# Kernel tuning notes

Measured on AMD Instinct MI355X. Metric: run time of the kernel, lower is better.

## Reference

```python
import jax, jax.numpy as jnp
import numpy as np
from jax import lax

# ---- static config (from BasePllay_2 / AdTopoLayer(out_features=50, T=25, m0=0.2, lims=[[224,0],[0,224]], K_max=2, p=0)) ----
H = W = 28
G = H * W
T = 25
K_MAX = 2
M0 = 0.2
OUT_FEATURES = 50
B = 32
TSEQ = jnp.linspace(0.0, 100.0, T)  # fixed landscape sample grid (covers DTM value range)

# static grid geometry from lims=[[224,0],[0,224]]
_xs = np.linspace(224.0, 0.0, H)
_ys = np.linspace(0.0, 224.0, W)
_pts = np.stack(np.meshgrid(_xs, _ys, indexing="ij"), -1).reshape(G, 2)
_d = np.sqrt(((_pts[:, None] - _pts[None]) ** 2).sum(-1))
_sidx = np.argsort(_d, axis=-1)
SDIST = jnp.asarray(np.take_along_axis(_d, _sidx, -1), jnp.float32)  # [G,G] sorted distances per grid point
SIDX = jnp.asarray(_sidx.astype(np.int32))                            # [G,G] static distance-sort order

# 4-connectivity neighbor table for the cubical (pixel) grid, -1 = invalid
_ii = np.arange(G).reshape(H, W)
_nb = np.full((H, W, 4), -1, np.int32)
_nb[1:, :, 0] = _ii[:-1, :]
_nb[:-1, :, 1] = _ii[1:, :]
_nb[:, 1:, 2] = _ii[:, :-1]
_nb[:, :-1, 3] = _ii[:, 1:]
NBR = jnp.asarray(_nb.reshape(G, 4))


def dtm(w):
    """Weighted distance-to-measure (r=2) on the fixed grid. w: [B,G] nonneg -> [B,G]."""
    sw = w[:, SIDX]                               # [B,G,G] weights in distance order
    cw = jnp.cumsum(sw, -1)
    d2 = SDIST ** 2
    cwd = jnp.cumsum(sw * d2[None], -1)
    bound = M0 * w.sum(-1)                        # [B]
    k = jnp.argmax(cw >= bound[:, None, None], -1)  # [B,G] first index reaching mass bound
    km1 = jnp.maximum(k - 1, 0)
    take = lambda a, i: jnp.take_along_axis(a, i[..., None], -1)[..., 0]
    has_prev = k > 0
    cw_p = jnp.where(has_prev, take(cw, km1), 0.0)
    cwd_p = jnp.where(has_prev, take(cwd, km1), 0.0)
    dk2 = d2[jnp.arange(G)[None, :], k]           # [B,G]
    val = (cwd_p + (bound[:, None] - cw_p) * dk2) / bound[:, None]
    return jnp.sqrt(jnp.maximum(val, 0.0))


def pd0(vals):
    """0-dim sublevel-set persistence of vals on the pixel grid (union-find, elder rule).
    Returns (births[G], deaths[G]); non-merging pixels yield zero-persistence pairs,
    essential components die at the max filtration value."""
    order = jnp.argsort(vals).astype(jnp.int32)
    rank = jnp.zeros(G, jnp.int32).at[order].set(jnp.arange(G, dtype=jnp.int32))

    def find(parent, i):
        return lax.while_loop(lambda j: parent[j] != j, lambda j: parent[j], i)

    def step(s, carry):
        parent, death = carry
        p = order[s]
        best = p
        for t in range(4):  # unrolled over the 4 grid neighbors (static)
            q = NBR[p, t]
            ok = (q >= 0) & (rank[jnp.maximum(q, 0)] < s)  # neighbor already inserted
            r = find(parent, jnp.where(ok, q, p))
            merge = ok & (r != best)
            r_old = rank[r] < rank[best]
            older = jnp.where(r_old, r, best)
            younger = jnp.where(r_old, best, r)
            widx = jnp.where(merge, younger, G)   # slot G is a dummy
            parent = parent.at[widx].set(older)
            death = death.at[widx].set(p)         # younger component dies at pixel p
            best = jnp.where(merge, older, best)
        return parent, death

    parent0 = jnp.arange(G + 1, dtype=jnp.int32)
    death0 = jnp.full(G + 1, -1, jnp.int32)
    _, death = lax.fori_loop(0, G, step, (parent0, death0))
    d = death[:G]
    deaths = jnp.where(d >= 0, vals[jnp.maximum(d, 0)], vals.max())
    return vals, deaths


def landscape(births, deaths):
    """K_MAX persistence landscapes sampled at TSEQ. [B,G] -> [B, K_MAX*T]."""
    tb = TSEQ[None, :, None] - births[:, None, :]   # [B,T,G]
    td = deaths[:, None, :] - TSEQ[None, :, None]
    tent = jnp.maximum(jnp.minimum(tb, td), 0.0)
    topk = lax.top_k(tent, K_MAX)[0]                # [B,T,K]
    return jnp.transpose(topk, (0, 2, 1)).reshape(births.shape[0], K_MAX * T)


def _forward(x, w_land, b_land, w_fc, b_fc):
    w = x.reshape(x.shape[0], -1)          # nn.Flatten: pixel intensities as measure weights
    v = dtm(w)                             # [B,G]
    births, deaths = jax.vmap(pd0)(v)
    feats = landscape(births, deaths)      # [B, 50]
    xt = feats @ w_land.T + b_land         # AdTopoLayer output [B, out_features]
    signal = jnp.abs(lax.stop_gradient(xt)).sum(0)   # torch: x.detach().abs().sum(0)
    out = jnp.maximum(xt, 0.0) @ w_fc.T + b_fc       # fc(relu(x))
    return out, signal

_forward_jit = jax.jit(_forward)


def setup_inputs() -> dict:
    key = jax.random.key(0)
    k = jax.random.split(key, 4)
    x = jax.random.uniform(k[0], (B, 1, H, W), jnp.float32)  # image-like nonneg weights
    w_land = jax.random.normal(k[1], (OUT_FEATURES, K_MAX * T), jnp.float32) * 0.1
    b_land = jnp.zeros((OUT_FEATURES,), jnp.float32)
    w_fc = jax.random.normal(k[2], (10, OUT_FEATURES), jnp.float32) * 0.1
    b_fc = jnp.zeros((10,), jnp.float32)
    return {"x": x, "w_land": w_land, "b_land": b_land, "w_fc": w_fc, "b_fc": b_fc}


def reference(x, w_land, b_land, w_fc, b_fc):
    return _forward_jit(x, w_land, b_land, w_fc, b_fc)
```

## Files before the change

### kernel.cpp

```cpp
#include <hip/hip_runtime.h>
#include <math.h>

#define H28 28
#define G784 784
#define BATCH 32
#define NOFF 3025
#define NOFFP 3072
#define NKEY 1459
#define TPTS 25
#define KMAX 2
#define NFEAT 50
#define OUTF 50
#define NCLS 10

#define NBX 16
#define BT 512
#define BT2 512
#define NWAVE (BT2 / 64)
#define HS 2048
#define EMAX 1024

struct OffPair { unsigned ij; float d2; };
struct OffTab  { OffPair e[NOFFP]; };

constexpr double csqrt(double x) {
  double r = x * 0.5 + 1.0;
  for (int i = 0; i < 20; i++) r = 0.5 * (r + x / r);
  return r;
}

constexpr OffTab make_offtab() {
  OffTab t{};
  int start[NKEY] = {};
  for (int i = 0; i < NOFF; i++) {
    int di = i / 55 - 27, dj = i % 55 - 27;
    start[di * di + dj * dj]++;
  }
  int run = 0;
  for (int k = 0; k < NKEY; k++) { int h = start[k]; start[k] = run; run += h; }
  for (int i = 0; i < NOFF; i++) {
    int di = i / 55 - 27, dj = i % 55 - 27;
    int key = di * di + dj * dj;
    int pos = start[key]++;
    float sd = (key == 0) ? 0.0f : (float)(csqrt((double)key) * (224.0 / 27.0));
    t.e[pos].ij = ((unsigned)(di & 0xffff)) | (((unsigned)(dj & 0xffff)) << 16);
    t.e[pos].d2 = sd * sd;
  }
  for (int i = NOFF; i < NOFFP; i++) { t.e[i].ij = 0x00640064u; t.e[i].d2 = 0.f; }
  return t;
}

__device__ constexpr OffTab OFFTAB = make_offtab();

__device__ __forceinline__ float wave_iscan_f32(float x) {
  int t;
  t = __builtin_amdgcn_update_dpp(0, __float_as_int(x), 0x111, 0xf, 0xf, true);
  x += __int_as_float(t);
  t = __builtin_amdgcn_update_dpp(0, __float_as_int(x), 0x112, 0xf, 0xf, true);
  x += __int_as_float(t);
  t = __builtin_amdgcn_update_dpp(0, __float_as_int(x), 0x114, 0xf, 0xf, true);
  x += __int_as_float(t);
  t = __builtin_amdgcn_update_dpp(0, __float_as_int(x), 0x118, 0xf, 0xf, true);
  x += __int_as_float(t);
  t = __builtin_amdgcn_update_dpp(0, __float_as_int(x), 0x142, 0xa, 0xf, true);
  x += __int_as_float(t);
  t = __builtin_amdgcn_update_dpp(0, __float_as_int(x), 0x143, 0xc, 0xf, true);
  x += __int_as_float(t);
  return x;
}

__global__ __launch_bounds__(BT) void dtm_kernel(const float* __restrict__ x,
                                                 float* __restrict__ v,
                                                 int* __restrict__ done_ctr) {
  __shared__ float w_s[G784];
  __shared__ float red[BT];

  const int tid = threadIdx.x;
  const int b   = blockIdx.x;
  const int bx  = blockIdx.y;

  if (b == 0 && bx == 0 && tid == 0) *done_ctr = 0;

  float ps = 0.f;
  for (int i = tid; i < G784; i += BT) {
    float wv = x[b * G784 + i];
    w_s[i] = wv;
    ps += wv;
  }
  red[tid] = ps;
  __syncthreads();
  if (tid < 256) red[tid] += red[tid + 256];
  __syncthreads();
  if (tid < 128) red[tid] += red[tid + 128];
  __syncthreads();
  if (tid < 64)  red[tid] += red[tid + 64];
  __syncthreads();
  if (tid < 64) {
    float vv = red[tid];
    vv += __shfl_down(vv, 32);
    vv += __shfl_down(vv, 16);
    vv += __shfl_down(vv, 8);
    vv += __shfl_down(vv, 4);
    vv += __shfl_down(vv, 2);
    vv += __shfl_down(vv, 1);
    if (tid == 0) red[0] = vv;
  }
  __syncthreads();
  const float bound = 0.2f * red[0];

  const int wave = tid >> 6;
  const int lane = tid & 63;
  const int slot = bx * 8 + wave;

  for (int g = slot; g < G784; g += NBX * 8) {
    const int i1 = g / H28, j1 = g % H28;
    float cw = 0.f, cwd = 0.f;
    float cwp = 0.f, cwdp = 0.f, dk2 = 0.f;
    bool crossed = false;
    int o = lane;
    unsigned ij = OFFTAB.e[o].ij;
    float d2v   = OFFTAB.e[o].d2;
    for (int base = 0; base < NOFFP && !crossed; base += 64) {
      int onext = o + 64;
      if (onext >= NOFFP) onext = o;
      const unsigned ij_n = OFFTAB.e[onext].ij;
      const float    d2_n = OFFTAB.e[onext].d2;
      const int di = (short)(ij & 0xffffu);
      const int dj = (short)(ij >> 16);
      const int i2 = i1 + di, j2 = j1 + dj;
      const bool inb = ((unsigned)i2 < (unsigned)H28) & ((unsigned)j2 < (unsigned)H28);
      const float wv = inb ? w_s[i2 * H28 + j2] : 0.f;
      const float wd = wv * d2v;
      const float psw = wave_iscan_f32(wv);
      const float psd = wave_iscan_f32(wd);
      const unsigned long long mask = __ballot(cw + psw >= bound);
      if (mask) {
        const int f = __ffsll((unsigned long long)mask) - 1;
        const float psw_f = __shfl(psw, f);
        const float w_f   = __shfl(wv, f);
        const float psd_f = __shfl(psd, f);
        const float wd_f  = __shfl(wd, f);
        dk2  = __shfl(d2v, f);
        cwp  = cw + (psw_f - w_f);
        cwdp = cwd + (psd_f - wd_f);
        crossed = true;
      } else {
        cw  += __int_as_float(__builtin_amdgcn_readlane(__float_as_int(psw), 63));
        cwd += __int_as_float(__builtin_amdgcn_readlane(__float_as_int(psd), 63));
      }
      ij = ij_n; d2v = d2_n; o = onext;
    }
    const float val = (cwdp + (bound - cwp) * dk2) / bound;
    if (lane == 0) v[b * G784 + g] = sqrtf(fmaxf(val, 0.f));
  }
}

__device__ __forceinline__ unsigned long long pix_key(const float* val_s, int p) {
  return (((unsigned long long)__float_as_uint(val_s[p])) << 10) | (unsigned)p;
}

__global__ __launch_bounds__(BT2) void pd0_kernel(const float* __restrict__ v,
                                                  float* __restrict__ feats,
                                                  int* __restrict__ done_ctr,
                                                  const float* __restrict__ w_land,
                                                  const float* __restrict__ b_land,
                                                  const float* __restrict__ w_fc,
                                                  const float* __restrict__ b_fc,
                                                  float* __restrict__ out) {
  __shared__ float val_s[G784];
  __shared__ int   ptr_s[G784];
  __shared__ int   parent[G784];
  __shared__ unsigned rank_s[G784];
  __shared__ unsigned claims[G784];
  __shared__ float deathv[G784];
  __shared__ int   mlist[G784];
  __shared__ unsigned long long oldkey[G784];
  __shared__ unsigned htag[HS];
  __shared__ unsigned long long hval[HS];
  __shared__ unsigned long long edges[EMAX];
  __shared__ float redf[NWAVE];
  __shared__ float wt1[NWAVE][TPTS];
  __shared__ float wt2[NWAVE][TPTS];
  __shared__ int   mcnt_sh, ecnt_sh, last_sh;
  __shared__ float vmax_sh;
  __shared__ float f_s[BATCH * NFEAT];
  __shared__ float xt_s[BATCH * OUTF];

  const int tid = threadIdx.x;
  const int b   = blockIdx.x;
  const int wave = tid >> 6;
  const int lane = tid & 63;
  if (tid == 0) { mcnt_sh = 0; ecnt_sh = 0; }

  for (int i = tid; i < HS; i += BT2) { htag[i] = 0u; hval[i] = ~0ULL; }

  float pm = -1e30f;
  for (int i = tid; i < G784; i += BT2) {
    float xv = v[b * G784 + i];
    val_s[i] = xv;
    pm = fmaxf(pm, xv);
    rank_s[i] = 0u;
    claims[i] = 0xFFFFFFFFu;
  }
  pm = fmaxf(pm, __shfl_down(pm, 32));
  pm = fmaxf(pm, __shfl_down(pm, 16));
  pm = fmaxf(pm, __shfl_down(pm, 8));
  pm = fmaxf(pm, __shfl_down(pm, 4));
  pm = fmaxf(pm, __shfl_down(pm, 2));
  pm = fmaxf(pm, __shfl_down(pm, 1));
  if (lane == 0) redf[wave] = pm;
  __syncthreads();
  if (tid == 0) {
    float m = redf[0];
    for (int w = 1; w < NWAVE; w++) m = fmaxf(m, redf[w]);
    vmax_sh = m;
  }
  __syncthreads();
  const float vmax = vmax_sh;

  for (int p = tid; p < G784; p += BT2) {
    unsigned long long kp = pix_key(val_s, p);
    int i = p / H28, j = p % H28;
    int nbs[4];
    nbs[0] = (i > 0)       ? p - H28 : -1;
    nbs[1] = (i < H28 - 1) ? p + H28 : -1;
    nbs[2] = (j > 0)       ? p - 1   : -1;
    nbs[3] = (j < H28 - 1) ? p + 1   : -1;
    int best = p;
    unsigned long long bk = kp;
    for (int t = 0; t < 4; t++) {
      int q = nbs[t];
      if (q >= 0) {
        unsigned long long kq = pix_key(val_s, q);
        if (kq < bk) { bk = kq; best = q; }
      }
    }
    ptr_s[p]  = best;
    parent[p] = p;
    deathv[p] = vmax;
    if (best == p) {
      oldkey[p] = kp;
      int mi = atomicAdd(&mcnt_sh, 1);
      mlist[mi] = p;
    }
  }
  __syncthreads();

  for (int r = 0; r < 5; r++) {
    for (int p = tid; p < G784; p += BT2) {
      int a = ptr_s[p];
      a = ptr_s[a];
      a = ptr_s[a];
      a = ptr_s[a];
      ptr_s[p] = a;
    }
    __syncthreads();
  }

  for (int p = tid; p < G784; p += BT2) {
    unsigned long long kp = pix_key(val_s, p);
    int i = p / H28, j = p % H28;
    int nbs[4];
    nbs[0] = (i > 0)       ? p - H28 : -1;
    nbs[1] = (i < H28 - 1) ? p + H28 : -1;
    nbs[2] = (j > 0)       ? p - 1   : -1;
    nbs[3] = (j < H28 - 1) ? p + 1   : -1;
    int bp = ptr_s[p];
    for (int t = 0; t < 4; t++) {
      int q = nbs[t];
      if (q >= 0) {
        unsigned long long kq = pix_key(val_s, q);
        int bq = ptr_s[q];
        if (kq < kp && bq != bp) {
          unsigned long long key =
              (((unsigned long long)__float_as_uint(val_s[p])) << 32) |
              (((unsigned long long)(unsigned)p) << 22) |
              (((unsigned long long)(unsigned)t) << 20) |
              (((unsigned long long)(unsigned)bp) << 10) |
              ((unsigned long long)(unsigned)bq);
          unsigned lo = (bp < bq) ? (unsigned)bp : (unsigned)bq;
          unsigned hi = (bp < bq) ? (unsigned)bq : (unsigned)bp;
          unsigned pairid = (lo << 10) | hi;
          unsigned idx = (pairid * 2654435761u) >> 21;
          for (;;) {
            unsigned t0 = atomicCAS(&htag[idx], 0u, pairid + 1u);
            if (t0 == 0u || t0 == pairid + 1u) { atomicMin(&hval[idx], key); break; }
            idx = (idx + 1) & (HS - 1);
          }
        }
      }
    }
  }
  __syncthreads();

  for (int i = tid; i < HS; i += BT2) {
    if (htag[i]) {
      int e = atomicAdd(&ecnt_sh, 1);
      if (e < EMAX) edges[e] = hval[i];
    }
  }
  __syncthreads();
  const int ne   = (ecnt_sh < EMAX) ? ecnt_sh : EMAX;
  const int mcnt = mcnt_sh;

  if (ne > 1 && ne <= BT2) {
    unsigned long long e = (tid < ne) ? edges[tid] : ~0ULL;
    __syncthreads();
    for (int kk = 2; kk <= BT2; kk <<= 1) {
      const bool up = ((tid & kk) == 0);
      for (int jj = kk >> 1; jj >= 64; jj >>= 1) {
        edges[tid] = e;
        __syncthreads();
        unsigned long long p = edges[tid ^ jj];
        __syncthreads();
        const bool lower = ((tid & jj) == 0);
        const bool keepmin = (up == lower);
        e = keepmin ? ((e < p) ? e : p) : ((e > p) ? e : p);
      }
      int jj0 = (kk >> 1 < 32) ? (kk >> 1) : 32;
      for (int jj = jj0; jj >= 1; jj >>= 1) {
        unsigned long long p = __shfl_xor((long long)e, jj, 64);
        const bool lower = ((tid & jj) == 0);
        const bool keepmin = (up == lower);
        e = keepmin ? ((e < p) ? e : p) : ((e > p) ? e : p);
      }
    }
    edges[tid] = e;
    __syncthreads();
  } else if (ne > 1) {
    int n2 = 1;
    while (n2 < ne) n2 <<= 1;
    for (int i = ne + tid; i < n2; i += BT2) edges[i] = ~0ULL;
    __syncthreads();
    for (int kk = 2; kk <= n2; kk <<= 1) {
      for (int jj = kk >> 1; jj > 0; jj >>= 1) {
        for (int i = tid; i < n2; i += BT2) {
          int ixj = i ^ jj;
          if (ixj > i) {
            unsigned long long a = edges[i], c = edges[ixj];
            bool up = ((i & kk) == 0);
            if ((a > c) == up) { edges[i] = c; edges[ixj] = a; }
          }
        }
        __syncthreads();
      }
    }
  }

  if (wave == 0) {
    int merged = 0;
    const int target = mcnt - 1;
    for (int base = 0; base < ne && merged < target; base += 64) {
      const int idx = base + lane;
      bool unresolved = (idx < ne);
      const unsigned long long e = unresolved ? edges[idx] : 0ULL;
      const int A  = (int)((e >> 10) & 1023u);
      const int Bq = (int)(e & 1023u);
      const float ev = __uint_as_float((unsigned)(e >> 32));
      for (;;) {
        int rA = A, rB = Bq;
        if (unresolved) {
          int xx = A;
          for (;;) { int p1 = parent[xx]; if (p1 == xx) break;
                     int p2 = parent[p1]; parent[xx] = p2; xx = p2; }
          rA = xx;
          xx = Bq;
          for (;;) { int p1 = parent[xx]; if (p1 == xx) break;
                     int p2 = parent[p1]; parent[xx] = p2; xx = p2; }
          rB = xx;
        }
        bool crossing = unresolved && (rA != rB);
        if (unresolved && !crossing) unresolved = false;
        if (__ballot(crossing) == 0ULL) break;
        if (crossing) {
          atomicMin(&claims[rA], (unsigned)lane);
          atomicMin(&claims[rB], (unsigned)lane);
        }
        __threadfence_block();
        bool win = crossing && claims[rA] == (unsigned)lane
                            && claims[rB] == (unsigned)lane;
        __threadfence_block();
        if (crossing) { claims[rA] = 0xFFFFFFFFu; claims[rB] = 0xFFFFFFFFu; }
        if (win) {
          unsigned long long ka = oldkey[rA], kb = oldkey[rB];
          unsigned ra_ = rank_s[rA], rb_ = rank_s[rB];
          int big   = (ra_ > rb_) ? rA : ((rb_ > ra_) ? rB : ((rA < rB) ? rA : rB));
          int small = (big == rA) ? rB : rA;
          parent[small] = big;
          if (ra_ == rb_) rank_s[big] = ra_ + 1u;
          unsigned long long okmin = (ka < kb) ? ka : kb;
          unsigned long long okmax = (ka < kb) ? kb : ka;
          oldkey[big] = okmin;
          int dying = (int)(okmax & 1023u);
          deathv[dying] = ev;
          unresolved = false;
        }
        __threadfence_block();
        merged += (int)__popcll(__ballot(win));
        if (merged >= target) break;
      }
    }
  }
  __syncthreads();

  if (lane < TPTS) {
    float ti = (float)((double)lane * (100.0 / 24.0));
    float t1 = 0.f, t2 = 0.f;
    for (int ii = wave; ii < mcnt; ii += NWAVE) {
      int m = mlist[ii];
      float tent = fminf(ti - val_s[m], deathv[m] - ti);
      tent = fmaxf(tent, 0.f);
      if (tent > t1)      { t2 = t1; t1 = tent; }
      else if (tent > t2) { t2 = tent; }
    }
    wt1[wave][lane] = t1;
    wt2[wave][lane] = t2;
  }
  __syncthreads();
  if (wave == 0 && lane < TPTS) {
    float t1 = 0.f, t2 = 0.f;
    for (int w = 0; w < NWAVE; w++) {
      float a = wt1[w][lane], c = wt2[w][lane];
      if (a >= t1) { t2 = fmaxf(t1, c); t1 = a; }
      else         { t2 = fmaxf(t2, a); }
    }
    feats[b * NFEAT + lane]        = t1;
    feats[b * NFEAT + TPTS + lane] = t2;
  }

  __threadfence();
  __syncthreads();
  if (tid == 0) last_sh = (atomicAdd(done_ctr, 1) == BATCH - 1) ? 1 : 0;
  __syncthreads();
  if (!last_sh) return;
  __threadfence();

  for (int i = tid; i < BATCH * NFEAT; i += BT2) f_s[i] = feats[i];
  __syncthreads();
  for (int idx = tid; idx < BATCH * OUTF; idx += BT2) {
    int bb = idx / OUTF, ff = idx % OUTF;
    float acc = b_land[ff];
    const float* wr = w_land + ff * NFEAT;
    const float* fr = f_s + bb * NFEAT;
    for (int j = 0; j < NFEAT; j++) acc += fr[j] * wr[j];
    xt_s[idx] = acc;
  }
  __syncthreads();
  if (tid < OUTF) {
    float s = 0.f;
    for (int bb = 0; bb < BATCH; bb++) s += fabsf(xt_s[bb * OUTF + tid]);
    out[BATCH * NCLS + tid] = s;
  }
  for (int idx = tid; idx < BATCH * NCLS; idx += BT2) {
    int bb = idx / NCLS, cc = idx % NCLS;
    float acc = b_fc[cc];
    const float* wr = w_fc + cc * OUTF;
    const float* xr = xt_s + bb * OUTF;
    for (int ff = 0; ff < OUTF; ff++) acc += fmaxf(xr[ff], 0.f) * wr[ff];
    out[bb * NCLS + cc] = acc;
  }
}

extern "C" void kernel_launch(void* const* d_in, const int* in_sizes, int n_in,
                              void* d_out, int out_size, void* d_ws, size_t ws_size,
                              hipStream_t stream) {
  (void)in_sizes; (void)n_in; (void)out_size; (void)ws_size;
  const float* x      = (const float*)d_in[0];
  const float* w_land = (const float*)d_in[1];
  const float* b_land = (const float*)d_in[2];
  const float* w_fc   = (const float*)d_in[3];
  const float* b_fc   = (const float*)d_in[4];
  float* out   = (float*)d_out;
  float* v     = (float*)d_ws;
  float* feats = v + BATCH * G784;
  int*   done  = (int*)(feats + BATCH * NFEAT);

  dim3 g1(BATCH, NBX);
  dtm_kernel<<<g1, BT, 0, stream>>>(x, v, done);
  pd0_kernel<<<BATCH, BT2, 0, stream>>>(v, feats, done,
                                        w_land, b_land, w_fc, b_fc, out);
}
```

Before: 101.8 us.

## Fuse DTM and persistence kernels via per-batch last-block-done counters

Merges the DTM and pd0 kernels into one launch: each of the NBX blocks per batch item computes its share of DTM values, then a per-batch atomic counter elects the last finishing block to run the union-find persistence and landscape for that item. The goal is to drop the second kernel launch and the grid-wide wait between the stages, so persistence for finished items overlaps with DTM work on others. Counters are padded per batch and cleared with a memset launch instead of in-kernel. The large shared-memory footprint now applies to every DTM block, which may lower occupancy. The in-register bitonic sort path is also generalized to any power-of-two size up to the block size.

Result: slower. 173.7 us (+70.7%).

```diff
diff --git a/kernel.cpp b/kernel.cpp
--- a/kernel.cpp
+++ b/kernel.cpp
@@ -15,10 +15,10 @@
 
 #define NBX 16
 #define BT 512
-#define BT2 512
-#define NWAVE (BT2 / 64)
+#define NWAVE (BT / 64)
 #define HS 2048
 #define EMAX 1024
+#define CSTRIDE 16
 
 struct OffPair { unsigned ij; float d2; };
 struct OffTab  { OffPair e[NOFFP]; };
@@ -69,17 +69,45 @@
   return x;
 }
 
-__global__ __launch_bounds__(BT) void dtm_kernel(const float* __restrict__ x,
-                                                 float* __restrict__ v,
-                                                 int* __restrict__ done_ctr) {
+__device__ __forceinline__ unsigned long long pix_key(const float* val_s, int p) {
+  return (((unsigned long long)__float_as_uint(val_s[p])) << 10) | (unsigned)p;
+}
+
+__global__ __launch_bounds__(BT) void fused_kernel(const float* __restrict__ x,
+                                                   float* __restrict__ v,
+                                                   float* __restrict__ feats,
+                                                   int* __restrict__ done,
+                                                   const float* __restrict__ w_land,
+                                                   const float* __restrict__ b_land,
+                                                   const float* __restrict__ w_fc,
+                                                   const float* __restrict__ b_fc,
+                                                   float* __restrict__ out) {
   __shared__ float w_s[G784];
   __shared__ float red[BT];
-
-  const int tid = threadIdx.x;
-  const int b   = blockIdx.x;
-  const int bx  = blockIdx.y;
-
-  if (b == 0 && bx == 0 && tid == 0) *done_ctr = 0;
+  __shared__ float val_s[G784];
+  __shared__ int   ptr_s[G784];
+  __shared__ int   parent[G784];
+  __shared__ unsigned rank_s[G784];
+  __shared__ unsigned claims[G784];
+  __shared__ float deathv[G784];
+  __shared__ int   mlist[G784];
+  __shared__ unsigned long long oldkey[G784];
+  __shared__ unsigned htag[HS];
+  __shared__ unsigned long long hval[HS];
+  __shared__ unsigned long long edges[EMAX];
+  __shared__ float redf[NWAVE];
+  __shared__ float wt1[NWAVE][TPTS];
+  __shared__ float wt2[NWAVE][TPTS];
+  __shared__ int   mcnt_sh, ecnt_sh, winner_sh, last_sh;
+  __shared__ float vmax_sh;
+  __shared__ float f_s[BATCH * NFEAT];
+  __shared__ float xt_s[BATCH * OUTF];
+
+  const int tid  = threadIdx.x;
+  const int b    = blockIdx.x;
+  const int bx   = blockIdx.y;
+  const int wave = tid >> 6;
+  const int lane = tid & 63;
 
   float ps = 0.f;
   for (int i = tid; i < G784; i += BT) {
@@ -108,10 +136,7 @@
   __syncthreads();
   const float bound = 0.2f * red[0];
 
-  const int wave = tid >> 6;
-  const int lane = tid & 63;
   const int slot = bx * 8 + wave;
-
   for (int g = slot; g < G784; g += NBX * 8) {
     const int i1 = g / H28, j1 = g % H28;
     float cw = 0.f, cwd = 0.f;
@@ -153,49 +178,22 @@
     const float val = (cwdp + (bound - cwp) * dk2) / bound;
     if (lane == 0) v[b * G784 + g] = sqrtf(fmaxf(val, 0.f));
   }
-}
-
-__device__ __forceinline__ unsigned long long pix_key(const float* val_s, int p) {
-  return (((unsigned long long)__float_as_uint(val_s[p])) << 10) | (unsigned)p;
-}
-
-__global__ __launch_bounds__(BT2) void pd0_kernel(const float* __restrict__ v,
-                                                  float* __restrict__ feats,
-                                                  int* __restrict__ done_ctr,
-                                                  const float* __restrict__ w_land,
-                                                  const float* __restrict__ b_land,
-                                                  const float* __restrict__ w_fc,
-                                                  const float* __restrict__ b_fc,
-                                                  float* __restrict__ out) {
-  __shared__ float val_s[G784];
-  __shared__ int   ptr_s[G784];
-  __shared__ int   parent[G784];
-  __shared__ unsigned rank_s[G784];
-  __shared__ unsigned claims[G784];
-  __shared__ float deathv[G784];
-  __shared__ int   mlist[G784];
-  __shared__ unsigned long long oldkey[G784];
-  __shared__ unsigned htag[HS];
-  __shared__ unsigned long long hval[HS];
-  __shared__ unsigned long long edges[EMAX];
-  __shared__ float redf[NWAVE];
-  __shared__ float wt1[NWAVE][TPTS];
-  __shared__ float wt2[NWAVE][TPTS];
-  __shared__ int   mcnt_sh, ecnt_sh, last_sh;
-  __shared__ float vmax_sh;
-  __shared__ float f_s[BATCH * NFEAT];
-  __shared__ float xt_s[BATCH * OUTF];
-
-  const int tid = threadIdx.x;
-  const int b   = blockIdx.x;
-  const int wave = tid >> 6;
-  const int lane = tid & 63;
-  if (tid == 0) { mcnt_sh = 0; ecnt_sh = 0; }
-
-  for (int i = tid; i < HS; i += BT2) { htag[i] = 0u; hval[i] = ~0ULL; }
+
+  __threadfence();
+  __syncthreads();
+  if (tid == 0) {
+    int old = atomicAdd(&done[b * CSTRIDE], 1);
+    winner_sh = (old == NBX - 1) ? 1 : 0;
+    mcnt_sh = 0; ecnt_sh = 0;
+  }
+  __syncthreads();
+  if (!winner_sh) return;
+  __threadfence();
+
+  for (int i = tid; i < HS; i += BT) { htag[i] = 0u; hval[i] = ~0ULL; }
 
   float pm = -1e30f;
-  for (int i = tid; i < G784; i += BT2) {
+  for (int i = tid; i < G784; i += BT) {
     float xv = v[b * G784 + i];
     val_s[i] = xv;
     pm = fmaxf(pm, xv);
@@ -218,7 +216,7 @@
   __syncthreads();
   const float vmax = vmax_sh;
 
-  for (int p = tid; p < G784; p += BT2) {
+  for (int p = tid; p < G784; p += BT) {
     unsigned long long kp = pix_key(val_s, p);
     int i = p / H28, j = p % H28;
     int nbs[4];
@@ -247,7 +245,7 @@
   __syncthreads();
 
   for (int r = 0; r < 5; r++) {
-    for (int p = tid; p < G784; p += BT2) {
+    for (int p = tid; p < G784; p += BT) {
       int a = ptr_s[p];
       a = ptr_s[a];
       a = ptr_s[a];
@@ -257,7 +255,7 @@
     __syncthreads();
   }
 
-  for (int p = tid; p < G784; p += BT2) {
+  for (int p = tid; p < G784; p += BT) {
     unsigned long long kp = pix_key(val_s, p);
     int i = p / H28, j = p % H28;
     int nbs[4];
@@ -293,7 +291,7 @@
   }
   __syncthreads();
 
-  for (int i = tid; i < HS; i += BT2) {
+  for (int i = tid; i < HS; i += BT) {
     if (htag[i]) {
       int e = atomicAdd(&ecnt_sh, 1);
       if (e < EMAX) edges[e] = hval[i];
@@ -303,46 +301,48 @@
   const int ne   = (ecnt_sh < EMAX) ? ecnt_sh : EMAX;
   const int mcnt = mcnt_sh;
 
-  if (ne > 1 && ne <= BT2) {
-    unsigned long long e = (tid < ne) ? edges[tid] : ~0ULL;
-    __syncthreads();
-    for (int kk = 2; kk <= BT2; kk <<= 1) {
-      const bool up = ((tid & kk) == 0);
-      for (int jj = kk >> 1; jj >= 64; jj >>= 1) {
-        edges[tid] = e;
-        __syncthreads();
-        unsigned long long p = edges[tid ^ jj];
-        __syncthreads();
-        const bool lower = ((tid & jj) == 0);
-        const bool keepmin = (up == lower);
-        e = keepmin ? ((e < p) ? e : p) : ((e > p) ? e : p);
-      }
-      int jj0 = (kk >> 1 < 32) ? (kk >> 1) : 32;
-      for (int jj = jj0; jj >= 1; jj >>= 1) {
-        unsigned long long p = __shfl_xor((long long)e, jj, 64);
-        const bool lower = ((tid & jj) == 0);
-        const bool keepmin = (up == lower);
-        e = keepmin ? ((e < p) ? e : p) : ((e > p) ? e : p);
-      }
-    }
-    edges[tid] = e;
-    __syncthreads();
-  } else if (ne > 1) {
+  if (ne > 1) {
     int n2 = 1;
     while (n2 < ne) n2 <<= 1;
-    for (int i = ne + tid; i < n2; i += BT2) edges[i] = ~0ULL;
-    __syncthreads();
-    for (int kk = 2; kk <= n2; kk <<= 1) {
-      for (int jj = kk >> 1; jj > 0; jj >>= 1) {
-        for (int i = tid; i < n2; i += BT2) {
-          int ixj = i ^ jj;
-          if (ixj > i) {
-            unsigned long long a = edges[i], c = edges[ixj];
-            bool up = ((i & kk) == 0);
-            if ((a > c) == up) { edges[i] = c; edges[ixj] = a; }
+    if (n2 <= BT) {
+      unsigned long long e = (tid < ne) ? edges[tid] : ~0ULL;
+      __syncthreads();
+      for (int kk = 2; kk <= n2; kk <<= 1) {
+        const bool up = ((tid & kk) == 0);
+        for (int jj = kk >> 1; jj >= 64; jj >>= 1) {
+          if (tid < n2) edges[tid] = e;
+          __syncthreads();
+          unsigned long long p = (tid < n2) ? edges[tid ^ jj] : ~0ULL;
+          __syncthreads();
+          const bool lower = ((tid & jj) == 0);
+          const bool keepmin = (up == lower);
+          if (tid < n2) e = keepmin ? ((e < p) ? e : p) : ((e > p) ? e : p);
+        }
+        int jj0 = (kk >> 1 < 32) ? (kk >> 1) : 32;
+        for (int jj = jj0; jj >= 1; jj >>= 1) {
+          unsigned long long p = __shfl_xor((long long)e, jj, 64);
+          const bool lower = ((tid & jj) == 0);
+          const bool keepmin = (up == lower);
+          if (tid < n2) e = keepmin ? ((e < p) ? e : p) : ((e > p) ? e : p);
+        }
+      }
+      if (tid < n2) edges[tid] = e;
+      __syncthreads();
+    } else {
+      for (int i = ne + tid; i < n2; i += BT) edges[i] = ~0ULL;
+      __syncthreads();
+      for (int kk = 2; kk <= n2; kk <<= 1) {
+        for (int jj = kk >> 1; jj > 0; jj >>= 1) {
+          for (int i = tid; i < n2; i += BT) {
+            int ixj = i ^ jj;
+            if (ixj > i) {
+              unsigned long long a = edges[i], c = edges[ixj];
+              bool up = ((i & kk) == 0);
+              if ((a > c) == up) { edges[i] = c; edges[ixj] = a; }
+            }
           }
-        }
-        __syncthreads();
+          __syncthreads();
+        }
       }
     }
   }
@@ -430,14 +430,14 @@
 
   __threadfence();
   __syncthreads();
-  if (tid == 0) last_sh = (atomicAdd(done_ctr, 1) == BATCH - 1) ? 1 : 0;
+  if (tid == 0) last_sh = (atomicAdd(&done[BATCH * CSTRIDE], 1) == BATCH - 1) ? 1 : 0;
   __syncthreads();
   if (!last_sh) return;
   __threadfence();
 
-  for (int i = tid; i < BATCH * NFEAT; i += BT2) f_s[i] = feats[i];
-  __syncthreads();
-  for (int idx = tid; idx < BATCH * OUTF; idx += BT2) {
+  for (int i = tid; i < BATCH * NFEAT; i += BT) f_s[i] = feats[i];
+  __syncthreads();
+  for (int idx = tid; idx < BATCH * OUTF; idx += BT) {
     int bb = idx / OUTF, ff = idx % OUTF;
     float acc = b_land[ff];
     const float* wr = w_land + ff * NFEAT;
@@ -451,7 +451,7 @@
     for (int bb = 0; bb < BATCH; bb++) s += fabsf(xt_s[bb * OUTF + tid]);
     out[BATCH * NCLS + tid] = s;
   }
-  for (int idx = tid; idx < BATCH * NCLS; idx += BT2) {
+  for (int idx = tid; idx < BATCH * NCLS; idx += BT) {
     int bb = idx / NCLS, cc = idx % NCLS;
     float acc = b_fc[cc];
     const float* wr = w_fc + cc * OUTF;
@@ -475,8 +475,9 @@
   float* feats = v + BATCH * G784;
   int*   done  = (int*)(feats + BATCH * NFEAT);
 
-  dim3 g1(BATCH, NBX);
-  dtm_kernel<<<g1, BT, 0, stream>>>(x, v, done);
-  pd0_kernel<<<BATCH, BT2, 0, stream>>>(v, feats, done,
-                                        w_land, b_land, w_fc, b_fc, out);
-}
+  hipMemsetAsync(done, 0, (BATCH + 1) * CSTRIDE * sizeof(int), stream);
+
+  dim3 g(BATCH, NBX);
+  fused_kernel<<<g, BT, 0, stream>>>(x, v, feats, done,
+                                     w_land, b_land, w_fc, b_fc, out);
+}
```
